# Kernel tuning notes

Measured on AMD Instinct MI355X. Metric: run time of the kernel, lower is better.

## Reference

```python
import jax, jax.numpy as jnp
from jax import lax
import numpy as np

DIM = 768
HEADS = 12
HD = DIM // HEADS  # 64
STRIDE = (1, 2, 2)
KER = (3, 3, 3)
PAD = [(1, 1), (1, 1), (1, 1)]
EPS = 1e-5


def _layernorm(x, g, b):
    mu = jnp.mean(x, axis=-1, keepdims=True)
    var = jnp.var(x, axis=-1, keepdims=True)
    return (x - mu) * lax.rsqrt(var + EPS) * g + b


def _attention_pool(t, wconv, g, b, T, H, W):
    # t: [B, heads, 1 + T*H*W, HD]; depthwise conv3d pooling on non-cls tokens
    B, Nh, _, Cd = t.shape
    cls_tok = t[:, :, :1, :]
    body = t[:, :, 1:, :].reshape(B * Nh, T, H, W, Cd).transpose(0, 4, 1, 2, 3)  # [BN, C, T, H, W]
    body = lax.conv_general_dilated(
        body, wconv, window_strides=STRIDE, padding=PAD,
        feature_group_count=Cd,
        dimension_numbers=('NCDHW', 'OIDHW', 'NCDHW'))
    Tp, Hp, Wp = body.shape[2], body.shape[3], body.shape[4]
    body = body.reshape(B, Nh, Cd, Tp * Hp * Wp).transpose(0, 1, 3, 2)  # [B, heads, Lp, C]
    t = jnp.concatenate([cls_tok, body], axis=2)
    t = _layernorm(t, g, b)
    return t, (Tp, Hp, Wp)


def setup_inputs() -> dict:
    key = jax.random.key(0)
    ks = jax.random.split(key, 12)
    T, H, W = 8, 28, 28
    B = 4
    N = 1 + T * H * W  # cls + thw tokens = 6273
    s = 0.02
    inp = {
        'x': jax.random.normal(ks[0], (B, N, DIM), jnp.float32),
        'qkv_w': jax.random.normal(ks[1], (DIM, 3 * DIM), jnp.float32) * s,
        'qkv_b': jnp.zeros((3 * DIM,), jnp.float32),
        'proj_w': jax.random.normal(ks[2], (DIM, DIM), jnp.float32) * s,
        'proj_b': jnp.zeros((DIM,), jnp.float32),
        'wq': jax.random.normal(ks[3], (HD, 1, 3, 3, 3), jnp.float32) * s,
        'wk': jax.random.normal(ks[4], (HD, 1, 3, 3, 3), jnp.float32) * s,
        'wv': jax.random.normal(ks[5], (HD, 1, 3, 3, 3), jnp.float32) * s,
        'gq': jnp.ones((HD,), jnp.float32), 'bq': jnp.zeros((HD,), jnp.float32),
        'gk': jnp.ones((HD,), jnp.float32), 'bk': jnp.zeros((HD,), jnp.float32),
        'gv': jnp.ones((HD,), jnp.float32), 'bv': jnp.zeros((HD,), jnp.float32),
        'thw_t': T, 'thw_h': H, 'thw_w': W,
    }
    return inp


def reference(x, qkv_w, qkv_b, proj_w, proj_b, wq, wk, wv,
              gq, bq, gk, bk, gv, bv, thw_t, thw_h, thw_w):
    B, N, C = x.shape
    scale = HD ** -0.5
    qkv = (x @ qkv_w + qkv_b).reshape(B, N, 3, HEADS, HD).transpose(2, 0, 3, 1, 4)
    q, k, v = qkv[0], qkv[1], qkv[2]  # [B, heads, N, HD]
    q, q_shape = _attention_pool(q, wq, gq, bq, thw_t, thw_h, thw_w)
    k, _ = _attention_pool(k, wk, gk, bk, thw_t, thw_h, thw_w)
    v, _ = _attention_pool(v, wv, gv, bv, thw_t, thw_h, thw_w)
    attn = jax.nn.softmax(jnp.einsum('bhqd,bhkd->bhqk', q, k) * scale, axis=-1)
    Nq = q.shape[2]
    out = jnp.einsum('bhqk,bhkd->bhqd', attn, v).transpose(0, 2, 1, 3).reshape(B, Nq, C)
    out = out @ proj_w + proj_b
    return out
```

## Files before the change

### kernel.cpp

```cpp
#include <hip/hip_runtime.h>
#include <hip/hip_bf16.h>

#define BB      4
#define NTOK    6273
#define NPOOL   1569
#define NPOOLP  1600
#define NHEADS  12
#define TT      8
#define HH      28
#define WW      28
#define HP      14
#define WP      14

typedef __attribute__((ext_vector_type(8))) _Float16 f16x8;
typedef __attribute__((ext_vector_type(4))) float f32x4;
typedef unsigned short u16;

#define AS1(p) ((const __attribute__((address_space(1))) void*)(p))
#define AS3(p) ((__attribute__((address_space(3))) void*)(p))

static __device__ __forceinline__ u16 f2h(float x) {
    union { _Float16 h; u16 u; } c; c.h = (_Float16)x; return c.u;
}
static __device__ __forceinline__ float h2f(u16 u) {
    union { u16 u; _Float16 h; } c; c.u = u; return (float)c.h;
}

__global__ __launch_bounds__(256) void cvt_f32_f16_kernel(
    const float* __restrict__ in, u16* __restrict__ out, int n4)
{
    int i = blockIdx.x * 256 + threadIdx.x;
    const int stride = gridDim.x * 256;
    for (; i < n4; i += stride) {
        const float4 v = ((const float4*)in)[i];
        ushort4 o;
        o.x = f2h(v.x); o.y = f2h(v.y); o.z = f2h(v.z); o.w = f2h(v.w);
        ((ushort4*)out)[i] = o;
    }
}

__global__ __launch_bounds__(256) void transpose_cvt_kernel(
    const float* __restrict__ W, u16* __restrict__ t, int K, int N)
{
    __shared__ float tile[32][33];
    const int n0 = blockIdx.x * 32, k0 = blockIdx.y * 32;
    const int tx = threadIdx.x, ty = threadIdx.y;
    #pragma unroll
    for (int i = 0; i < 4; ++i)
        tile[ty + i * 8][tx] = W[(size_t)(k0 + ty + i * 8) * N + n0 + tx];
    __syncthreads();
    #pragma unroll
    for (int i = 0; i < 4; ++i) {
        const int n = n0 + ty + i * 8;
        t[(size_t)n * K + k0 + tx] = f2h(tile[tx][ty + i * 8]);
    }
}

__global__ __launch_bounds__(256) void wt_transpose_kernel(
    const float* __restrict__ wq, const float* __restrict__ wk,
    const float* __restrict__ wv, u16* __restrict__ wTh)
{
    const int which = blockIdx.x;
    const float* w = (which == 0) ? wq : (which == 1) ? wk : wv;
    u16* o = wTh + which * 27 * 64;
    for (int i = threadIdx.x; i < 27 * 64; i += 256) {
        const int j = i >> 6, d = i & 63;
        o[j * 64 + d] = f2h(w[d * 27 + j]);
    }
}

#define GBK 32
#define GNKT 24

__global__ __launch_bounds__(512, 4) void gemm256_qkv_kernel(
    const u16* __restrict__ Af, const u16* __restrict__ Bt,
    const float* __restrict__ bias, int M,
    u16* __restrict__ o0, u16* __restrict__ o1, u16* __restrict__ o2)
{
    __shared__ __align__(16) u16 A_s[2][256 * GBK];
    __shared__ __align__(16) u16 B_s[2][128 * GBK];

    const int tid  = threadIdx.x;
    const int lane = tid & 63;
    const int w    = tid >> 6;
    const int wr   = w >> 1, wc = w & 1;

    const int nwg = gridDim.x;
    const int qch = nwg >> 3, rch = nwg & 7;
    const int xcd = blockIdx.x & 7, idx = blockIdx.x >> 3;
    const int wg  = (xcd < rch ? xcd * (qch + 1) : rch * (qch + 1) + (xcd - rch) * qch) + idx;
    const int m0 = (wg / 18) * 256;
    const int nb = wg % 18;
    const int n0 = nb * 128;

    const int rA0 = tid >> 2;
    const int cA0 = ((tid & 3) ^ ((rA0 >> 1) & 3)) << 3;
    const int ch1 = 512 + tid;
    const int rA1 = ch1 >> 2;
    const int cA1 = ((ch1 & 3) ^ ((rA1 >> 1) & 3)) << 3;
    const u16* pA0 = Af + (size_t)min(m0 + rA0, M - 1) * 768 + cA0;
    const u16* pA1 = Af + (size_t)min(m0 + rA1, M - 1) * 768 + cA1;
    const u16* pB  = Bt + (size_t)(n0 + rA0) * 768 + cA0;
    const int dstA0 = (w * 64) * 8;
    const int dstA1 = (512 + w * 64) * 8;
    const int dstB  = (w * 64) * 8;

    #define STAGE(buf, kk) do { \
        __builtin_amdgcn_global_load_lds(AS1(pA0 + (kk)), AS3(&A_s[buf][dstA0]), 16, 0, 0); \
        __builtin_amdgcn_global_load_lds(AS1(pA1 + (kk)), AS3(&A_s[buf][dstA1]), 16, 0, 0); \
        __builtin_amdgcn_global_load_lds(AS1(pB  + (kk)), AS3(&B_s[buf][dstB ]), 16, 0, 0); \
    } while (0)

    STAGE(0, 0);

    f32x4 acc[4][4] = {};
    const int fr = lane & 15, fq = lane >> 4;
    const int sw8 = (fq ^ ((fr >> 1) & 3)) << 3;

    for (int t = 0; t < GNKT; ++t) {
        const int cur = t & 1;
        if (t < GNKT - 1) {
            STAGE(cur ^ 1, (t + 1) * GBK);
            asm volatile("s_waitcnt vmcnt(3)" ::: "memory");
        } else {
            asm volatile("s_waitcnt vmcnt(0)" ::: "memory");
        }
        __builtin_amdgcn_s_barrier();

        f16x8 a[4], b[4];
        #pragma unroll
        for (int m = 0; m < 4; ++m)
            a[m] = *(const f16x8*)&A_s[cur][(wr * 64 + m * 16 + fr) * GBK + sw8];
        #pragma unroll
        for (int n = 0; n < 4; ++n)
            b[n] = *(const f16x8*)&B_s[cur][(wc * 64 + n * 16 + fr) * GBK + sw8];

        __builtin_amdgcn_s_setprio(1);
        #pragma unroll
        for (int m = 0; m < 4; ++m)
            #pragma unroll
            for (int n = 0; n < 4; ++n)
                acc[m][n] = __builtin_amdgcn_mfma_f32_16x16x32_f16(a[m], b[n], acc[m][n], 0, 0, 0);
        __builtin_amdgcn_s_setprio(0);

        if (t < GNKT - 1) __builtin_amdgcn_s_barrier();
    }
    #undef STAGE

    const int s = nb / 6;
    u16* const dsts = (s == 0) ? o0 : (s == 1) ? o1 : o2;
    #pragma unroll
    for (int m = 0; m < 4; ++m) {
        const int growb = m0 + wr * 64 + m * 16 + fq * 4;
        #pragma unroll
        for (int j = 0; j < 4; ++j) {
            const int grow = growb + j;
            if (grow >= M) continue;
            const int bidx = grow / NTOK;
            const int ntok = grow - bidx * NTOK;
            #pragma unroll
            for (int n = 0; n < 4; ++n) {
                const int gcol = n0 + wc * 64 + n * 16 + fr;
                const float v = acc[m][n][j] + bias[gcol];
                const int rem = gcol - s * 768;
                const int h = rem >> 6, d = rem & 63;
                dsts[(size_t)((bidx * NHEADS + h) * NTOK + ntok) * 64 + d] = f2h(v);
            }
        }
    }
}

template<int NBLK, bool QKV, typename OutT>
__global__ __launch_bounds__(512) void gemm_fp16_kernel(
    const u16* __restrict__ Af, const u16* __restrict__ Bt,
    const float* __restrict__ bias, int M,
    OutT* __restrict__ o0, OutT* __restrict__ o1, OutT* __restrict__ o2)
{
    __shared__ __align__(16) u16 A_s[128 * 32];
    __shared__ __align__(16) u16 B_s[128 * 32];

    const int tid  = threadIdx.x;
    const int lane = tid & 63;
    const int w    = tid >> 6;
    const int wr   = w >> 2, wc = w & 3;

    const int nwg = gridDim.x;
    const int qch = nwg >> 3, rch = nwg & 7;
    const int xcd = blockIdx.x & 7, idx = blockIdx.x >> 3;
    const int wg  = (xcd < rch ? xcd * (qch + 1) : rch * (qch + 1) + (xcd - rch) * qch) + idx;
    const int m0 = (wg / NBLK) * 128;
    const int n0 = (wg % NBLK) * 128;

    f32x4 acc[4][2] = {};

    const int srow   = lane >> 2;
    const int sslot  = (lane & 3) ^ ((srow >> 1) & 3);

    for (int kt = 0; kt < 24; ++kt) {
        const int k0 = kt * 32;
        __syncthreads();

        {
            const int rb = w * 16;
            const int ra = min(m0 + rb + srow, M - 1);
            __builtin_amdgcn_global_load_lds(AS1(Af + (size_t)ra * 768 + k0 + sslot * 8),
                                             AS3(&A_s[rb * 32]), 16, 0, 0);
            __builtin_amdgcn_global_load_lds(AS1(Bt + (size_t)(n0 + rb + srow) * 768 + k0 + sslot * 8),
                                             AS3(&B_s[rb * 32]), 16, 0, 0);
        }
        __syncthreads();

        const int fr = lane & 15, fq = lane >> 4;
        const int rslot = (fq ^ ((fr >> 1) & 3)) << 3;
        f16x8 a[4], b[2];
        #pragma unroll
        for (int m = 0; m < 4; ++m)
            a[m] = *(const f16x8*)&A_s[(wr * 64 + m * 16 + fr) * 32 + rslot];
        #pragma unroll
        for (int n = 0; n < 2; ++n)
            b[n] = *(const f16x8*)&B_s[(wc * 32 + n * 16 + fr) * 32 + rslot];

        #pragma unroll
        for (int m = 0; m < 4; ++m)
            #pragma unroll
            for (int n = 0; n < 2; ++n)
                acc[m][n] = __builtin_amdgcn_mfma_f32_16x16x32_f16(a[m], b[n], acc[m][n], 0, 0, 0);
    }

    const int fr = lane & 15, fq = lane >> 4;
    #pragma unroll
    for (int m = 0; m < 4; ++m) {
        const int grow_base = m0 + wr * 64 + m * 16 + fq * 4;
        #pragma unroll
        for (int j = 0; j < 4; ++j) {
            const int grow = grow_base + j;
            if (grow >= M) continue;
            int b = 0, ntok = 0;
            if (QKV) { b = grow / NTOK; ntok = grow - b * NTOK; }
            #pragma unroll
            for (int n = 0; n < 2; ++n) {
                const int gcol = n0 + wc * 32 + n * 16 + fr;
                const float v = acc[m][n][j] + bias[gcol];
                if (QKV) {
                    const int s = gcol / 768;
                    const int rem = gcol - s * 768;
                    const int h = rem >> 6, d = rem & 63;
                    OutT* dst = (s == 0) ? o0 : (s == 1) ? o1 : o2;
                    dst[(size_t)((b * NHEADS + h) * NTOK + ntok) * 64 + d] = (OutT)f2h(v);
                } else {
                    o0[(size_t)grow * (NBLK * 128) + gcol] = (OutT)v;
                }
            }
        }
    }
}

#define PL_PG  50
#define PL_NWG (3 * 48 * PL_PG)
__global__ __launch_bounds__(256) void pool_ln_kernel(
    const u16* __restrict__ qr, const u16* __restrict__ kr, const u16* __restrict__ vr,
    const u16* __restrict__ wTh,
    const float* __restrict__ gq, const float* __restrict__ bq,
    const float* __restrict__ gk, const float* __restrict__ bk,
    const float* __restrict__ gv, const float* __restrict__ bv,
    u16* __restrict__ qph, u16* __restrict__ kph, u16* __restrict__ vpt)
{
    const int wg = (blockIdx.x & 7) * (PL_NWG / 8) + (blockIdx.x >> 3);
    const int which = wg / (48 * PL_PG);
    const int rem   = wg - which * (48 * PL_PG);
    const int bh    = rem / PL_PG;
    const int pg    = rem - bh * PL_PG;
    const int wv_   = threadIdx.x >> 6;
    const int lane  = threadIdx.x & 63;
    const int tg    = lane >> 3;
    const int d0    = (lane & 7) * 8;

    const int p  = pg * 32 + wv_ * 8 + tg;
    const int pc = min(p, NPOOL - 1);

    const u16*   in  = (which == 0) ? qr : (which == 1) ? kr : vr;
    const u16*   wTb = wTh + which * 27 * 64;
    const float* g   = (which == 0) ? gq : (which == 1) ? gk : gv;
    const float* bb_ = (which == 0) ? bq : (which == 1) ? bk : bv;
    const float qscale = (which == 0) ? 0.125f : 1.0f;

    const size_t inb = (size_t)bh * NTOK * 64;

    float s[8] = {};
    if (pc == 0) {
        const f16x8 t = *(const f16x8*)&in[inb + d0];
        #pragma unroll
        for (int c = 0; c < 8; ++c) s[c] = (float)t[c];
    } else {
        const int idx = pc - 1;
        const int tp = idx / (HP * WP);
        const int r2 = idx - tp * (HP * WP);
        const int hp = r2 / WP;
        const int wp = r2 - hp * WP;

        const f16x8 z8 = (f16x8)(_Float16)0.0f;
        #pragma unroll
        for (int kt = 0; kt < 3; ++kt) {
            const int it = tp + kt - 1;
            #pragma unroll
            for (int kh = 0; kh < 3; ++kh) {
                const int ih = hp * 2 + kh - 1;
                #pragma unroll
                for (int kw = 0; kw < 3; ++kw) {
                    const int iw = wp * 2 + kw - 1;
                    const int j  = kt * 9 + kh * 3 + kw;
                    const bool ok = (it >= 0) & (it < TT) & (ih >= 0) & (ih < HH) &
                                    (iw >= 0) & (iw < WW);
                    const int n   = 1 + (it * HH + ih) * WW + iw;
                    const int n_c = ok ? n : 0;
                    const f16x8 tv  = *(const f16x8*)&in[inb + (size_t)n_c * 64 + d0];
                    const f16x8 wv8 = *(const f16x8*)&wTb[j * 64 + d0];
                    const f16x8 ts  = ok ? tv : z8;
                    #pragma unroll
                    for (int c = 0; c < 8; ++c)
                        s[c] = fmaf((float)wv8[c], (float)ts[c], s[c]);
                }
            }
        }
    }

    float sum = 0.f, ssq = 0.f;
    #pragma unroll
    for (int c = 0; c < 8; ++c) { sum += s[c]; ssq += s[c] * s[c]; }
    #pragma unroll
    for (int off = 1; off < 8; off <<= 1) {
        sum += __shfl_xor(sum, off);
        ssq += __shfl_xor(ssq, off);
    }
    const float mu  = sum * (1.f / 64.f);
    const float var = ssq * (1.f / 64.f) - mu * mu;
    const float rs  = rsqrtf(var + 1e-5f);

    float g8[8], b8[8];
    {
        const float4 g0 = *(const float4*)&g[d0];
        const float4 g1 = *(const float4*)&g[d0 + 4];
        const float4 b0 = *(const float4*)&bb_[d0];
        const float4 b1 = *(const float4*)&bb_[d0 + 4];
        g8[0]=g0.x; g8[1]=g0.y; g8[2]=g0.z; g8[3]=g0.w;
        g8[4]=g1.x; g8[5]=g1.y; g8[6]=g1.z; g8[7]=g1.w;
        b8[0]=b0.x; b8[1]=b0.y; b8[2]=b0.z; b8[3]=b0.w;
        b8[4]=b1.x; b8[5]=b1.y; b8[6]=b1.z; b8[7]=b1.w;
    }

    u16 oo[8];
    #pragma unroll
    for (int c = 0; c < 8; ++c)
        oo[c] = f2h(((s[c] - mu) * rs * g8[c] + b8[c]) * qscale);

    if (which == 2) {
        u16* base = vpt + (size_t)bh * 64 * NPOOLP + p;
        if (p < NPOOL) {
            #pragma unroll
            for (int c = 0; c < 8; ++c)
                base[(size_t)(d0 + c) * NPOOLP] = oo[c];
        } else {
            #pragma unroll
            for (int c = 0; c < 8; ++c)
                base[(size_t)(d0 + c) * NPOOLP] = 0;
        }
    } else if (p < NPOOL) {
        u16* out = (which == 0) ? qph : kph;
        u16* dst = &out[((size_t)bh * NPOOL + p) * 64 + d0];
        *(ushort4*)&dst[0] = *(ushort4*)&oo[0];
        *(ushort4*)&dst[4] = *(ushort4*)&oo[4];
    }
}

__global__ __launch_bounds__(256) void flash_attn_fp16_kernel(
    const u16* __restrict__ qh, const u16* __restrict__ kh,
    const u16* __restrict__ vt, float* __restrict__ accf,
    float* __restrict__ lf)
{
    __shared__ __align__(16) u16 K_s[64 * 64];
    __shared__ __align__(16) u16 V_s[64 * 64];
    __shared__ __align__(16) u16 P_s[4][32 * 64];

    const int bh = blockIdx.y;
    const int q0 = blockIdx.x * 128;
    const int z  = blockIdx.z;
    const int kt_lo = z ? 13 : 0, kt_hi = z ? 25 : 13;
    const int tid = threadIdx.x;
    const int w = tid >> 6, lane = tid & 63;
    const int fr = lane & 15, fq = lane >> 4;
    const int l8 = lane >> 3;
    const int sw = 8 * ((lane & 7) ^ l8);

    const size_t hb  = (size_t)bh * NPOOL * 64;
    const size_t vtb = (size_t)bh * 64 * NPOOLP;
    float* accb = accf + (size_t)z * BB * NPOOL * 768;
    float* lb   = lf   + (size_t)z * 48 * NPOOL;

    f16x8 qf_[2][2];
    #pragma unroll
    for (int qf = 0; qf < 2; ++qf) {
        const int row = min(q0 + w * 32 + qf * 16 + fr, NPOOL - 1);
        #pragma unroll
        for (int half = 0; half < 2; ++half)
            qf_[qf][half] = *(const f16x8*)&qh[hb + (size_t)row * 64 + half * 32 + fq * 8];
    }

    f16x8 ones;
    #pragma unroll
    for (int i = 0; i < 8; ++i) ones[i] = (_Float16)1.0f;

    f32x4 acc[2][4] = {};
    f32x4 l_acc[2] = {};

    #define LDSW(buf, row, colbyte) \
        (*(const f16x8*)((const char*)(buf) + ((row) * 128 + ((colbyte) ^ (((row) & 7) << 4)))))

    for (int kt = kt_lo; kt < kt_hi; ++kt) {
        const int k0 = kt * 64;
        __syncthreads();

        #pragma unroll
        for (int i = 0; i < 2; ++i) {
            const int rb = w * 16 + i * 8;
            const int r  = rb + l8;
            const int gk = min(k0 + r, NPOOL - 1);
            __builtin_amdgcn_global_load_lds(AS1(kh + hb + (size_t)gk * 64 + sw),
                                             AS3(&K_s[rb * 64]), 16, 0, 0);
            __builtin_amdgcn_global_load_lds(AS1(vt + vtb + (size_t)r * NPOOLP + k0 + sw),
                                             AS3(&V_s[rb * 64]), 16, 0, 0);
        }
        __syncthreads();

        f32x4 sv[2][4];
        #pragma unroll
        for (int nf = 0; nf < 4; ++nf) {
            const int krow = nf * 16 + fr;
            const f16x8 kf0 = LDSW(K_s, krow, fq * 16);
            const f16x8 kf1 = LDSW(K_s, krow, 64 + fq * 16);
            #pragma unroll
            for (int qf = 0; qf < 2; ++qf) {
                f32x4 s = {};
                s = __builtin_amdgcn_mfma_f32_16x16x32_f16(qf_[qf][0], kf0, s, 0, 0, 0);
                s = __builtin_amdgcn_mfma_f32_16x16x32_f16(qf_[qf][1], kf1, s, 0, 0, 0);
                sv[qf][nf] = s;
            }
        }

        #pragma unroll
        for (int nf = 0; nf < 4; ++nf) {
            const bool valid = (k0 + nf * 16 + fr) < NPOOL;
            #pragma unroll
            for (int qf = 0; qf < 2; ++qf) {
                #pragma unroll
                for (int j = 0; j < 4; ++j) {
                    const float p = valid ? __expf(sv[qf][nf][j]) : 0.f;
                    const int row = qf * 16 + fq * 4 + j;
                    const int bo  = row * 128 + ((nf * 32 + fr * 2) ^ ((row & 7) << 4));
                    *(u16*)((char*)&P_s[w][0] + bo) = f2h(p);
                }
            }
        }
        __builtin_amdgcn_sched_barrier(0);

        f16x8 pa[2][2];
        #pragma unroll
        for (int qf = 0; qf < 2; ++qf) {
            const int prow = qf * 16 + fr;
            pa[qf][0] = LDSW(&P_s[w][0], prow, fq * 16);
            pa[qf][1] = LDSW(&P_s[w][0], prow, 64 + fq * 16);
            l_acc[qf] = __builtin_amdgcn_mfma_f32_16x16x32_f16(pa[qf][0], ones, l_acc[qf], 0, 0, 0);
            l_acc[qf] = __builtin_amdgcn_mfma_f32_16x16x32_f16(pa[qf][1], ones, l_acc[qf], 0, 0, 0);
        }
        #pragma unroll
        for (int df = 0; df < 4; ++df) {
            const int vrow = df * 16 + fr;
            const f16x8 v0 = LDSW(V_s, vrow, fq * 16);
            const f16x8 v1 = LDSW(V_s, vrow, 64 + fq * 16);
            acc[0][df] = __builtin_amdgcn_mfma_f32_16x16x32_f16(pa[0][0], v0, acc[0][df], 0, 0, 0);
            acc[0][df] = __builtin_amdgcn_mfma_f32_16x16x32_f16(pa[0][1], v1, acc[0][df], 0, 0, 0);
            acc[1][df] = __builtin_amdgcn_mfma_f32_16x16x32_f16(pa[1][0], v0, acc[1][df], 0, 0, 0);
            acc[1][df] = __builtin_amdgcn_mfma_f32_16x16x32_f16(pa[1][1], v1, acc[1][df], 0, 0, 0);
        }
    }
    #undef LDSW

    const int b = bh / NHEADS, h = bh % NHEADS;
    #pragma unroll
    for (int qf = 0; qf < 2; ++qf) {
        #pragma unroll
        for (int j = 0; j < 4; ++j) {
            const int q = q0 + w * 32 + qf * 16 + fq * 4 + j;
            if (q >= NPOOL) continue;
            float* dst = &accb[((size_t)b * NPOOL + q) * 768 + h * 64];
            #pragma unroll
            for (int df = 0; df < 4; ++df)
                dst[df * 16 + fr] = acc[qf][df][j];
            if (fr == 0)
                lb[(size_t)bh * NPOOL + q] = l_acc[qf][j];
        }
    }
}

__global__ __launch_bounds__(256) void combine_kernel(
    const float* __restrict__ acc0, const float* __restrict__ acc1,
    const float* __restrict__ l0, const float* __restrict__ l1,
    u16* __restrict__ aoh)
{
    const int n4 = BB * NPOOL * 768 / 4;
    int i = blockIdx.x * 256 + threadIdx.x;
    const int stride = gridDim.x * 256;
    for (; i < n4; i += stride) {
        const int e0  = i * 4;
        const int row = e0 / 768;
        const int c   = e0 - row * 768;
        const int b   = row / NPOOL;
        const int q   = row - b * NPOOL;
        const int h   = c >> 6;
        const size_t li = (size_t)(b * NHEADS + h) * NPOOL + q;
        const float inv = 1.f / (l0[li] + l1[li]);
        const float4 a0 = ((const float4*)acc0)[i];
        const float4 a1 = ((const float4*)acc1)[i];
        ushort4 o;
        o.x = f2h((a0.x + a1.x) * inv);
        o.y = f2h((a0.y + a1.y) * inv);
        o.z = f2h((a0.z + a1.z) * inv);
        o.w = f2h((a0.w + a1.w) * inv);
        ((ushort4*)aoh)[i] = o;
    }
}

extern "C" void kernel_launch(void* const* d_in, const int* in_sizes, int n_in,
                              void* d_out, int out_size, void* d_ws, size_t ws_size,
                              hipStream_t stream)
{
    const float* x      = (const float*)d_in[0];
    const float* qkv_w  = (const float*)d_in[1];
    const float* qkv_b  = (const float*)d_in[2];
    const float* proj_w = (const float*)d_in[3];
    const float* proj_b = (const float*)d_in[4];
    const float* wq     = (const float*)d_in[5];
    const float* wk     = (const float*)d_in[6];
    const float* wv     = (const float*)d_in[7];
    const float* gq     = (const float*)d_in[8];
    const float* bq     = (const float*)d_in[9];
    const float* gk     = (const float*)d_in[10];
    const float* bk     = (const float*)d_in[11];
    const float* gv     = (const float*)d_in[12];
    const float* bv     = (const float*)d_in[13];

    const size_t RAW  = (size_t)BB * NHEADS * NTOK * 64;
    const size_t PLD  = (size_t)BB * NHEADS * NPOOL * 64;
    const size_t VTSZ = (size_t)BB * NHEADS * 64 * NPOOLP;
    const size_t AOSZ = (size_t)BB * NPOOL * 768;

    u16* q_raw = (u16*)d_ws;
    u16* k_raw = q_raw + RAW;
    u16* v_raw = k_raw + RAW;
    u16* xh    = v_raw + RAW;
    u16* qph   = xh + RAW;
    u16* kph   = qph + PLD;
    u16* vpb   = kph + PLD;
    u16* vpt   = vpb + PLD;
    u16* wth   = vpt + VTSZ;
    u16* pwth  = wth + (size_t)2304 * 768;
    u16* wTh   = pwth + (size_t)768 * 768;
    float* acc0 = (float*)(wTh + 3 * 27 * 64);
    float* acc1 = acc0 + AOSZ;
    float* l0   = acc1 + AOSZ;
    float* l1   = l0 + (size_t)48 * NPOOL;
    u16* aoh   = q_raw;

    cvt_f32_f16_kernel<<<2048, 256, 0, stream>>>(x, xh, (int)(RAW / 4));

    transpose_cvt_kernel<<<dim3(2304 / 32, 768 / 32), dim3(32, 8), 0, stream>>>(
        qkv_w, wth, 768, 2304);
    transpose_cvt_kernel<<<dim3(768 / 32, 768 / 32), dim3(32, 8), 0, stream>>>(
        proj_w, pwth, 768, 768);
    wt_transpose_kernel<<<3, 256, 0, stream>>>(wq, wk, wv, wTh);

    gemm256_qkv_kernel<<<dim3(99 * 18), 512, 0, stream>>>(
        xh, wth, qkv_b, BB * NTOK, q_raw, k_raw, v_raw);

    pool_ln_kernel<<<dim3(PL_NWG), 256, 0, stream>>>(
        q_raw, k_raw, v_raw, wTh, gq, bq, gk, bk, gv, bv,
        qph, kph, vpt);

    flash_attn_fp16_kernel<<<dim3(13, 48, 2), 256, 0, stream>>>(
        qph, kph, vpt, acc0, l0);

    combine_kernel<<<2048, 256, 0, stream>>>(acc0, acc1, l0, l1, aoh);

    gemm_fp16_kernel<6, false, float><<<dim3(50 * 6), 512, 0, stream>>>(
        aoh, pwth, proj_b, BB * NPOOL, (float*)d_out, nullptr, nullptr);
}
```

Baseline: 307.0 us.

## Drop split-K flash attention and combine kernel; use 64-row query tiles

```diff
diff --git a/kernel.cpp b/kernel.cpp
--- a/kernel.cpp
+++ b/kernel.cpp
@@ -374,17 +374,14 @@
 
 __global__ __launch_bounds__(256) void flash_attn_fp16_kernel(
     const u16* __restrict__ qh, const u16* __restrict__ kh,
-    const u16* __restrict__ vt, float* __restrict__ accf,
-    float* __restrict__ lf)
+    const u16* __restrict__ vt, u16* __restrict__ aoh)
 {
     __shared__ __align__(16) u16 K_s[64 * 64];
     __shared__ __align__(16) u16 V_s[64 * 64];
-    __shared__ __align__(16) u16 P_s[4][32 * 64];
+    __shared__ __align__(16) u16 P_s[4][16 * 64];
 
     const int bh = blockIdx.y;
-    const int q0 = blockIdx.x * 128;
-    const int z  = blockIdx.z;
-    const int kt_lo = z ? 13 : 0, kt_hi = z ? 25 : 13;
+    const int q0 = blockIdx.x * 64;
     const int tid = threadIdx.x;
     const int w = tid >> 6, lane = tid & 63;
     const int fr = lane & 15, fq = lane >> 4;
@@ -393,29 +390,26 @@
 
     const size_t hb  = (size_t)bh * NPOOL * 64;
     const size_t vtb = (size_t)bh * 64 * NPOOLP;
-    float* accb = accf + (size_t)z * BB * NPOOL * 768;
-    float* lb   = lf   + (size_t)z * 48 * NPOOL;
-
-    f16x8 qf_[2][2];
-    #pragma unroll
-    for (int qf = 0; qf < 2; ++qf) {
-        const int row = min(q0 + w * 32 + qf * 16 + fr, NPOOL - 1);
+
+    f16x8 qf_[2];
+    {
+        const int row = min(q0 + w * 16 + fr, NPOOL - 1);
         #pragma unroll
         for (int half = 0; half < 2; ++half)
-            qf_[qf][half] = *(const f16x8*)&qh[hb + (size_t)row * 64 + half * 32 + fq * 8];
+            qf_[half] = *(const f16x8*)&qh[hb + (size_t)row * 64 + half * 32 + fq * 8];
     }
 
     f16x8 ones;
     #pragma unroll
     for (int i = 0; i < 8; ++i) ones[i] = (_Float16)1.0f;
 
-    f32x4 acc[2][4] = {};
-    f32x4 l_acc[2] = {};
+    f32x4 acc[4] = {};
+    f32x4 l_acc = {};
 
     #define LDSW(buf, row, colbyte) \
         (*(const f16x8*)((const char*)(buf) + ((row) * 128 + ((colbyte) ^ (((row) & 7) << 4)))))
 
-    for (int kt = kt_lo; kt < kt_hi; ++kt) {
+    for (int kt = 0; kt < 25; ++kt) {
         const int k0 = kt * 64;
         __syncthreads();
 
@@ -431,101 +425,56 @@
         }
         __syncthreads();
 
-        f32x4 sv[2][4];
+        f32x4 sv[4];
         #pragma unroll
         for (int nf = 0; nf < 4; ++nf) {
             const int krow = nf * 16 + fr;
             const f16x8 kf0 = LDSW(K_s, krow, fq * 16);
             const f16x8 kf1 = LDSW(K_s, krow, 64 + fq * 16);
-            #pragma unroll
-            for (int qf = 0; qf < 2; ++qf) {
-                f32x4 s = {};
-                s = __builtin_amdgcn_mfma_f32_16x16x32_f16(qf_[qf][0], kf0, s, 0, 0, 0);
-                s = __builtin_amdgcn_mfma_f32_16x16x32_f16(qf_[qf][1], kf1, s, 0, 0, 0);
-                sv[qf][nf] = s;
-            }
+            f32x4 s = {};
+            s = __builtin_amdgcn_mfma_f32_16x16x32_f16(qf_[0], kf0, s, 0, 0, 0);
+            s = __builtin_amdgcn_mfma_f32_16x16x32_f16(qf_[1], kf1, s, 0, 0, 0);
+            sv[nf] = s;
         }
 
         #pragma unroll
         for (int nf = 0; nf < 4; ++nf) {
             const bool valid = (k0 + nf * 16 + fr) < NPOOL;
             #pragma unroll
-            for (int qf = 0; qf < 2; ++qf) {
-                #pragma unroll
-                for (int j = 0; j < 4; ++j) {
-                    const float p = valid ? __expf(sv[qf][nf][j]) : 0.f;
-                    const int row = qf * 16 + fq * 4 + j;
-                    const int bo  = row * 128 + ((nf * 32 + fr * 2) ^ ((row & 7) << 4));
-                    *(u16*)((char*)&P_s[w][0] + bo) = f2h(p);
-                }
+            for (int j = 0; j < 4; ++j) {
+                const float p = valid ? __expf(sv[nf][j]) : 0.f;
+                const int row = fq * 4 + j;
+                const int bo  = row * 128 + ((nf * 32 + fr * 2) ^ ((row & 7) << 4));
+                *(u16*)((char*)&P_s[w][0] + bo) = f2h(p);
             }
         }
         __builtin_amdgcn_sched_barrier(0);
 
-        f16x8 pa[2][2];
-        #pragma unroll
-        for (int qf = 0; qf < 2; ++qf) {
-            const int prow = qf * 16 + fr;
-            pa[qf][0] = LDSW(&P_s[w][0], prow, fq * 16);
-            pa[qf][1] = LDSW(&P_s[w][0], prow, 64 + fq * 16);
-            l_acc[qf] = __builtin_amdgcn_mfma_f32_16x16x32_f16(pa[qf][0], ones, l_acc[qf], 0, 0, 0);
-            l_acc[qf] = __builtin_amdgcn_mfma_f32_16x16x32_f16(pa[qf][1], ones, l_acc[qf], 0, 0, 0);
-        }
+        const f16x8 pa0 = LDSW(&P_s[w][0], fr, fq * 16);
+        const f16x8 pa1 = LDSW(&P_s[w][0], fr, 64 + fq * 16);
+        l_acc = __builtin_amdgcn_mfma_f32_16x16x32_f16(pa0, ones, l_acc, 0, 0, 0);
+        l_acc = __builtin_amdgcn_mfma_f32_16x16x32_f16(pa1, ones, l_acc, 0, 0, 0);
         #pragma unroll
         for (int df = 0; df < 4; ++df) {
             const int vrow = df * 16 + fr;
             const f16x8 v0 = LDSW(V_s, vrow, fq * 16);
             const f16x8 v1 = LDSW(V_s, vrow, 64 + fq * 16);
-            acc[0][df] = __builtin_amdgcn_mfma_f32_16x16x32_f16(pa[0][0], v0, acc[0][df], 0, 0, 0);
-            acc[0][df] = __builtin_amdgcn_mfma_f32_16x16x32_f16(pa[0][1], v1, acc[0][df], 0, 0, 0);
-            acc[1][df] = __builtin_amdgcn_mfma_f32_16x16x32_f16(pa[1][0], v0, acc[1][df], 0, 0, 0);
-            acc[1][df] = __builtin_amdgcn_mfma_f32_16x16x32_f16(pa[1][1], v1, acc[1][df], 0, 0, 0);
+            acc[df] = __builtin_amdgcn_mfma_f32_16x16x32_f16(pa0, v0, acc[df], 0, 0, 0);
+            acc[df] = __builtin_amdgcn_mfma_f32_16x16x32_f16(pa1, v1, acc[df], 0, 0, 0);
         }
     }
     #undef LDSW
 
     const int b = bh / NHEADS, h = bh % NHEADS;
     #pragma unroll
-    for (int qf = 0; qf < 2; ++qf) {
-        #pragma unroll
-        for (int j = 0; j < 4; ++j) {
-            const int q = q0 + w * 32 + qf * 16 + fq * 4 + j;
-            if (q >= NPOOL) continue;
-            float* dst = &accb[((size_t)b * NPOOL + q) * 768 + h * 64];
-            #pragma unroll
-            for (int df = 0; df < 4; ++df)
-                dst[df * 16 + fr] = acc[qf][df][j];
-            if (fr == 0)
-                lb[(size_t)bh * NPOOL + q] = l_acc[qf][j];
-        }
-    }
-}
-
-__global__ __launch_bounds__(256) void combine_kernel(
-    const float* __restrict__ acc0, const float* __restrict__ acc1,
-    const float* __restrict__ l0, const float* __restrict__ l1,
-    u16* __restrict__ aoh)
-{
-    const int n4 = BB * NPOOL * 768 / 4;
-    int i = blockIdx.x * 256 + threadIdx.x;
-    const int stride = gridDim.x * 256;
-    for (; i < n4; i += stride) {
-        const int e0  = i * 4;
-        const int row = e0 / 768;
-        const int c   = e0 - row * 768;
-        const int b   = row / NPOOL;
-        const int q   = row - b * NPOOL;
-        const int h   = c >> 6;
-        const size_t li = (size_t)(b * NHEADS + h) * NPOOL + q;
-        const float inv = 1.f / (l0[li] + l1[li]);
-        const float4 a0 = ((const float4*)acc0)[i];
-        const float4 a1 = ((const float4*)acc1)[i];
-        ushort4 o;
-        o.x = f2h((a0.x + a1.x) * inv);
-        o.y = f2h((a0.y + a1.y) * inv);
-        o.z = f2h((a0.z + a1.z) * inv);
-        o.w = f2h((a0.w + a1.w) * inv);
-        ((ushort4*)aoh)[i] = o;
+    for (int j = 0; j < 4; ++j) {
+        const int q = q0 + w * 16 + fq * 4 + j;
+        if (q >= NPOOL) continue;
+        const float inv = 1.f / l_acc[j];
+        u16* dst = &aoh[((size_t)(b * NPOOL + q)) * 768 + h * 64];
+        #pragma unroll
+        for (int df = 0; df < 4; ++df)
+            dst[df * 16 + fr] = f2h(acc[df][j] * inv);
     }
 }
 
@@ -564,10 +513,6 @@
     u16* wth   = vpt + VTSZ;
     u16* pwth  = wth + (size_t)2304 * 768;
     u16* wTh   = pwth + (size_t)768 * 768;
-    float* acc0 = (float*)(wTh + 3 * 27 * 64);
-    float* acc1 = acc0 + AOSZ;
-    float* l0   = acc1 + AOSZ;
-    float* l1   = l0 + (size_t)48 * NPOOL;
     u16* aoh   = q_raw;
 
     cvt_f32_f16_kernel<<<2048, 256, 0, stream>>>(x, xh, (int)(RAW / 4));
@@ -585,10 +530,8 @@
         q_raw, k_raw, v_raw, wTh, gq, bq, gk, bk, gv, bv,
         qph, kph, vpt);
 
-    flash_attn_fp16_kernel<<<dim3(13, 48, 2), 256, 0, stream>>>(
-        qph, kph, vpt, acc0, l0);
-
-    combine_kernel<<<2048, 256, 0, stream>>>(acc0, acc1, l0, l1, aoh);
+    flash_attn_fp16_kernel<<<dim3(25, 48), 256, 0, stream>>>(
+        qph, kph, vpt, aoh);
 
     gemm_fp16_kernel<6, false, float><<<dim3(50 * 6), 512, 0, stream>>>(
         aoh, pwth, proj_b, BB * NPOOL, (float*)d_out, nullptr, nullptr);
```

Measured after the change: 296.8 us. 1.03x faster.
